# Performance work log

Measured on AMD Instinct MI355X. Metric: run time of the kernel, lower is better.

The kernel has to match this reference:

```python
import jax, jax.numpy as jnp
import numpy as np

B, L, H, D = 2, 2048, 16, 64
E = H * D  # 1024

def setup_inputs() -> dict:
    key = jax.random.key(0)
    k1, k2, k3 = jax.random.split(key, 3)
    net_in = jax.random.normal(k1, (B, L, E), dtype=jnp.float32)
    # torch nn.Linear weights are [out_features, in_features]; scale like kaiming-uniform-ish
    W_qkv = jax.random.normal(k2, (3 * E, E), dtype=jnp.float32) * (1.0 / np.sqrt(E))
    W_out = jax.random.normal(k3, (E, E), dtype=jnp.float32) * (1.0 / np.sqrt(E))
    return {"net_in": net_in, "W_qkv": W_qkv, "W_out": W_out}

def reference(net_in, W_qkv, W_out):
    b, l, c = net_in.shape
    h, d = H, D
    # c_proj: x @ W_qkv.T -> (B, L, 3E), split into q, k, v
    qkv = jnp.einsum('blc,ec->ble', net_in, W_qkv)
    q, k, v = jnp.split(qkv, 3, axis=-1)
    # reshape to (B, H, L, D)
    q = q.reshape(b, l, h, d).transpose(0, 2, 1, 3)
    k = k.reshape(b, l, h, d).transpose(0, 2, 1, 3)
    v = v.reshape(b, l, h, d).transpose(0, 2, 1, 3)
    scale = 1.0 / np.sqrt(d).astype(np.float32)
    attn = jnp.einsum('bhqd,bhkd->bhqk', q, k) * scale  # (B, H, L, L)
    causal = jnp.tril(jnp.ones((l, l), dtype=bool))
    attn = jnp.where(causal[None, None, :, :], attn, -jnp.inf)
    attn = jax.nn.softmax(attn, axis=-1)
    out = jnp.einsum('bhqk,bhkd->bhqd', attn, v)  # (B, H, L, D)
    out = out.transpose(0, 2, 1, 3).reshape(b, l, c)
    return jnp.einsum('blc,ec->ble', out, W_out)
```

## Files before the change

### kernel.cpp

```cpp
#include <hip/hip_runtime.h>
#include <hip/hip_bf16.h>

#define LOG2E 1.44269504088896340736f

typedef __attribute__((ext_vector_type(8))) short s16x8;
typedef __attribute__((ext_vector_type(4))) short s16x4;
typedef __attribute__((ext_vector_type(2))) unsigned int u32x2;
typedef __attribute__((ext_vector_type(4))) float f32x4;
typedef __attribute__((ext_vector_type(16))) float f32x16;

__device__ inline short f2bf(float f) {
  __hip_bfloat16 h = __float2bfloat16(f);
  union { __hip_bfloat16 h; short s; } u; u.h = h; return u.s;
}

__device__ inline void gl_lds16(const void* g, void* l) {
  __builtin_amdgcn_global_load_lds(
      (const __attribute__((address_space(1))) void*)g,
      (__attribute__((address_space(3))) void*)l, 16, 0, 0);
}

__global__ __launch_bounds__(256)
void cvt_all(const float* __restrict__ Wqkv, const float* __restrict__ Wout,
             const float* __restrict__ net,
             short* __restrict__ dWqkv, short* __restrict__ dWout,
             short* __restrict__ dnet) {
  int bid = blockIdx.x;
  const float* src; short* dst; int i;
  if (bid < 3072)      { src = Wqkv; dst = dWqkv; i = bid * 256 + threadIdx.x; }
  else if (bid < 4096) { src = Wout; dst = dWout; i = (bid - 3072) * 256 + threadIdx.x; }
  else                 { src = net;  dst = dnet;  i = (bid - 4096) * 256 + threadIdx.x; }
  f32x4 v = ((const f32x4*)src)[i];
  s16x4 o;
  o[0] = f2bf(v[0]); o[1] = f2bf(v[1]); o[2] = f2bf(v[2]); o[3] = f2bf(v[3]);
  ((s16x4*)dst)[i] = o;
}

template<int OUTF32, int VTRANS, int SPLITK, int NSUB>
__global__ __launch_bounds__(256)
void gemm128(const short* __restrict__ A, int lda,
             const short* __restrict__ B, int ldb,
             void* __restrict__ Cp, int ldc, int Klen,
             short* __restrict__ P1) {
  int id = (int)(blockIdx.x + (blockIdx.y << 5));
  int xcd = id & 7, slot = id >> 3;
  int m0, n0;
  if constexpr (NSUB == 3) {
    int g = slot / 12, r = slot - g * 12;
    m0 = (g * 4 + (r & 3)) * 128;
    n0 = (xcd * 3 + (r >> 2)) * 128;
  } else {
    m0 = (slot & 31) * 128;
    n0 = (xcd * NSUB + (slot >> 5)) * 128;
  }
  int kbeg = SPLITK ? (int)blockIdx.z * Klen : 0;
  int t = threadIdx.x;
  int w = t >> 6, lane = t & 63;
  int l16 = lane & 15, quad = lane >> 4;
  int wm = w >> 1, wn = w & 1;

  __shared__ __align__(16) short As[2][128 * 32];
  __shared__ __align__(16) short Bs[2][128 * 32];

  int scell = ((t & 3) ^ ((t >> 3) & 3)) * 8;
  const short* bsrc = B + (size_t)(n0 + (t >> 2)) * ldb + kbeg + scell;
  const short* asrc = A + (size_t)(m0 + (t >> 2)) * lda + kbeg + scell;
  int rcell = (quad ^ ((l16 >> 1) & 3)) * 8;

  f32x4 acc[4][4];
#pragma unroll
  for (int i = 0; i < 4; ++i)
#pragma unroll
    for (int j = 0; j < 4; ++j) acc[i][j] = (f32x4){0.f, 0.f, 0.f, 0.f};

#pragma unroll
  for (int r = 0; r < 2; ++r) {
    gl_lds16(asrc + (size_t)r * 64 * lda, (char*)As + r * 4096 + w * 1024);
    gl_lds16(bsrc + (size_t)r * 64 * ldb, (char*)Bs + r * 4096 + w * 1024);
  }

  int nks = Klen >> 5;
  for (int ks = 0; ks < nks; ++ks) {
    int cur = ks & 1;
    if (ks + 1 < nks) {
      int k0 = (ks + 1) * 32;
      int nb = cur ^ 1;
#pragma unroll
      for (int r = 0; r < 2; ++r) {
        gl_lds16(asrc + k0 + (size_t)r * 64 * lda, (char*)As + nb * 8192 + r * 4096 + w * 1024);
        gl_lds16(bsrc + k0 + (size_t)r * 64 * ldb, (char*)Bs + nb * 8192 + r * 4096 + w * 1024);
      }
      asm volatile("s_waitcnt vmcnt(4)" ::: "memory");
    } else {
      asm volatile("s_waitcnt vmcnt(0)" ::: "memory");
    }
    asm volatile("s_barrier" ::: "memory");

    s16x8 af[4], bf[4];
#pragma unroll
    for (int i = 0; i < 4; ++i) {
      af[i] = *(const s16x8*)(As[cur] + (wm * 64 + i * 16 + l16) * 32 + rcell);
      bf[i] = *(const s16x8*)(Bs[cur] + (wn * 64 + i * 16 + l16) * 32 + rcell);
    }
#pragma unroll
    for (int i = 0; i < 4; ++i)
#pragma unroll
      for (int j = 0; j < 4; ++j)
        acc[i][j] = __builtin_amdgcn_mfma_f32_16x16x32_bf16(af[i], bf[j], acc[i][j], 0, 0, 0);

    asm volatile("s_barrier" ::: "memory");
  }

  if (SPLITK && blockIdx.z == 1) {
#pragma unroll
    for (int i = 0; i < 4; ++i)
#pragma unroll
      for (int j = 0; j < 4; ++j)
#pragma unroll
        for (int rr = 0; rr < 4; ++rr) {
          size_t row = m0 + wm * 64 + i * 16 + quad * 4 + rr;
          size_t col = n0 + wn * 64 + j * 16 + l16;
          float* fp = (float*)(P1 + row * 3072 + 1024);
          fp[col] = acc[i][j][rr];
        }
  } else if (VTRANS && n0 >= 2048) {
    short* Cs = (short*)Cp;
#pragma unroll
    for (int i = 0; i < 4; ++i)
#pragma unroll
      for (int j = 0; j < 4; ++j) {
        int colg = n0 + wn * 64 + j * 16 + l16;
        int d = colg & 63;
        size_t dst = (size_t)(m0 + wm * 64 + d) * ldc + (colg - d) + i * 16 + quad * 4;
        s16x4 ob;
#pragma unroll
        for (int rr = 0; rr < 4; ++rr) ob[rr] = f2bf(acc[i][j][rr]);
        *(s16x4*)(Cs + dst) = ob;
      }
  } else {
#pragma unroll
    for (int i = 0; i < 4; ++i)
#pragma unroll
      for (int j = 0; j < 4; ++j)
#pragma unroll
        for (int rr = 0; rr < 4; ++rr) {
          size_t row = m0 + wm * 64 + i * 16 + quad * 4 + rr;
          size_t col = n0 + wn * 64 + j * 16 + l16;
          if (OUTF32) ((float*)Cp)[row * ldc + col] = acc[i][j][rr];
          else        ((short*)Cp)[row * ldc + col] = f2bf(acc[i][j][rr]);
        }
  }
}

__global__ __launch_bounds__(256)
void reduce_add(float* __restrict__ out, const short* __restrict__ qkv) {
  int row = blockIdx.x;
  int c = threadIdx.x;
  const f32x4* p = (const f32x4*)(qkv + (size_t)row * 3072 + 1024);
  f32x4* o = (f32x4*)(out + (size_t)row * 1024);
  f32x4 v = o[c];
  f32x4 q = p[c];
  v[0] += q[0]; v[1] += q[1]; v[2] += q[2]; v[3] += q[3];
  o[c] = v;
}

__global__ __launch_bounds__(256, 4)
void attn(short* __restrict__ qkv) {
  const int L = 2048, E3 = 3072, EO = 1024;
  int id = (int)(blockIdx.x + (blockIdx.y << 5));
  int xcd = id & 7;
  int s = id >> 3;
  int bh = xcd * 4 + (s & 3);
  int u = s >> 2;
  int vv = u & 15;
  int qidx = (u & 16) ? (31 - vv) : vv;
  int b = bh >> 4, h = bh & 15;
  int q0 = qidx * 64;
  int t = threadIdx.x;
  int wave = t >> 6, lane = t & 63;
  int qh = wave >> 1, kh = wave & 1;
  int l31 = lane & 31, hsel = lane >> 5;
  int khi4 = hsel * 4;
  int key = (lane >> 1) & 3;
  const float SENT = -3.0e38f;
  const float SC = 0.125f * LOG2E;

  __shared__ __align__(16) short Ks[2][2][64][32];
  __shared__ __align__(16) short Vt[2][2][64][32];

  int rowbase = b * L;

  s16x8 qf[4];
  {
    const short* qp = qkv + (size_t)(rowbase + q0 + qh * 32 + l31) * E3 + h * 64 + hsel * 8;
#pragma unroll
    for (int e = 0; e < 4; ++e) {
      s16x8 raw = *(const s16x8*)(qp + e * 16);
#pragma unroll
      for (int j = 0; j < 8; ++j) {
        union { float f; int i; } u2; u2.i = ((int)(unsigned short)raw[j]) << 16;
        raw[j] = f2bf(u2.f * SC);
      }
      qf[e] = raw;
    }
  }

  int scell = ((lane & 3) ^ ((lane >> 3) & 3)) * 8;
  const short* ksrc = qkv + (size_t)(rowbase + wave * 16 + (lane >> 2)) * E3 + EO
                      + h * 64 + scell;
  const short* vsrc = qkv + (size_t)(rowbase + wave * 16 + (lane >> 2)) * E3 + 2 * EO
                      + h * 64 + scell;

  float l_acc = 0.f;
  f32x16 o0 = (f32x16){0.f,0.f,0.f,0.f,0.f,0.f,0.f,0.f,0.f,0.f,0.f,0.f,0.f,0.f,0.f,0.f};
  f32x16 o1 = o0;

  int nkb = qidx + 1;

  gl_lds16(ksrc,      (char*)Ks + wave * 1024);
  gl_lds16(ksrc + 32, (char*)Ks + 4096 + wave * 1024);
  gl_lds16(vsrc,      (char*)Vt + wave * 1024);
  gl_lds16(vsrc + 32, (char*)Vt + 4096 + wave * 1024);

  for (int kb = 0; kb < nkb; ++kb) {
    int cur = kb & 1;
    __syncthreads();
    if (kb + 1 < nkb) {
      size_t koff = (size_t)((kb + 1) * 64) * E3;
      int nb = cur ^ 1;
      gl_lds16(ksrc + koff,      (char*)Ks + nb * 8192 + wave * 1024);
      gl_lds16(ksrc + koff + 32, (char*)Ks + nb * 8192 + 4096 + wave * 1024);
      gl_lds16(vsrc + koff,      (char*)Vt + nb * 8192 + wave * 1024);
      gl_lds16(vsrc + koff + 32, (char*)Vt + nb * 8192 + 4096 + wave * 1024);
    }

    int rel = (q0 + qh * 32) - (kb * 64 + kh * 32);
    if (rel > -32) {
      int krow = kh * 32 + l31;
      s16x8 kf0 = *(const s16x8*)(&Ks[cur][0][krow][((0 + hsel) ^ key) * 8]);
      s16x8 kf1 = *(const s16x8*)(&Ks[cur][0][krow][((2 + hsel) ^ key) * 8]);
      s16x8 kf2 = *(const s16x8*)(&Ks[cur][1][krow][((0 + hsel) ^ key) * 8]);
      s16x8 kf3 = *(const s16x8*)(&Ks[cur][1][krow][((2 + hsel) ^ key) * 8]);
      s16x8 vf00 = *(const s16x8*)(&Vt[cur][kh][ 0 + l31][((0 + hsel) ^ key) * 8]);
      s16x8 vf01 = *(const s16x8*)(&Vt[cur][kh][32 + l31][((0 + hsel) ^ key) * 8]);
      s16x8 vf10 = *(const s16x8*)(&Vt[cur][kh][ 0 + l31][((2 + hsel) ^ key) * 8]);
      s16x8 vf11 = *(const s16x8*)(&Vt[cur][kh][32 + l31][((2 + hsel) ^ key) * 8]);

      f32x16 sf = (f32x16){0.f,0.f,0.f,0.f,0.f,0.f,0.f,0.f,0.f,0.f,0.f,0.f,0.f,0.f,0.f,0.f};
      sf = __builtin_amdgcn_mfma_f32_32x32x16_bf16(kf0, qf[0], sf, 0, 0, 0);
      sf = __builtin_amdgcn_mfma_f32_32x32x16_bf16(kf1, qf[1], sf, 0, 0, 0);
      sf = __builtin_amdgcn_mfma_f32_32x32x16_bf16(kf2, qf[2], sf, 0, 0, 0);
      sf = __builtin_amdgcn_mfma_f32_32x32x16_bf16(kf3, qf[3], sf, 0, 0, 0);

      if (rel < 31) {
        int thr = rel + l31 - khi4;
#pragma unroll
        for (int r = 0; r < 16; ++r) {
          const int base_k = (r & 3) + 8 * (r >> 2);
          if (base_k > thr) sf[r] = SENT;
        }
      }

      float pv[16];
#pragma unroll
      for (int r = 0; r < 16; ++r) {
        pv[r] = __builtin_amdgcn_exp2f(sf[r]);
        l_acc += pv[r];
      }

#define PKW(lo, hi) __builtin_amdgcn_perm(__float_as_uint(hi) + 0x8000u, \
                                          __float_as_uint(lo) + 0x8000u, 0x07060302u)
      unsigned A0 = PKW(pv[0],  pv[1]),  A1 = PKW(pv[2],  pv[3]);
      unsigned B0 = PKW(pv[4],  pv[5]),  B1 = PKW(pv[6],  pv[7]);
      unsigned C0 = PKW(pv[8],  pv[9]),  C1 = PKW(pv[10], pv[11]);
      unsigned D0 = PKW(pv[12], pv[13]), D1 = PKW(pv[14], pv[15]);
#undef PKW
      u32x2 sw0 = __builtin_amdgcn_permlane32_swap(A0, B0, false, false);
      u32x2 sw1 = __builtin_amdgcn_permlane32_swap(A1, B1, false, false);
      u32x2 sw2 = __builtin_amdgcn_permlane32_swap(C0, D0, false, false);
      u32x2 sw3 = __builtin_amdgcn_permlane32_swap(C1, D1, false, false);
      union { s16x8 v; unsigned u[4]; } P0, P1;
      P0.u[0] = sw0[0]; P0.u[1] = sw1[0]; P0.u[2] = sw0[1]; P0.u[3] = sw1[1];
      P1.u[0] = sw2[0]; P1.u[1] = sw3[0]; P1.u[2] = sw2[1]; P1.u[3] = sw3[1];

      o0 = __builtin_amdgcn_mfma_f32_32x32x16_bf16(vf00, P0.v, o0, 0, 0, 0);
      o0 = __builtin_amdgcn_mfma_f32_32x32x16_bf16(vf10, P1.v, o0, 0, 0, 0);
      o1 = __builtin_amdgcn_mfma_f32_32x32x16_bf16(vf01, P0.v, o1, 0, 0, 0);
      o1 = __builtin_amdgcn_mfma_f32_32x32x16_bf16(vf11, P1.v, o1, 0, 0, 0);
    }
  }

  l_acc += __shfl_xor(l_acc, 32);
  __syncthreads();
  float* fs = (float*)&Ks[0][0][0][0];
  float* lb = (float*)&Vt[0][0][0][0];
  if (kh) {
#pragma unroll
    for (int r = 0; r < 16; ++r) {
      fs[qh * 2048 + r * 64 + lane] = o0[r];
      fs[qh * 2048 + (16 + r) * 64 + lane] = o1[r];
    }
    if (lane < 32) lb[qh * 32 + lane] = l_acc;
  }
  __syncthreads();
  if (!kh) {
    float inv = 1.f / (l_acc + lb[qh * 32 + l31]);
    size_t obase = (size_t)(rowbase + q0 + qh * 32 + l31) * E3 + h * 64;
    int fb = qh * 2048;
#pragma unroll
    for (int g = 0; g < 4; ++g) {
      s16x4 w0, w1;
#pragma unroll
      for (int rr = 0; rr < 4; ++rr) {
        int r = g * 4 + rr;
        w0[rr] = f2bf((o0[r] + fs[fb + r * 64 + lane]) * inv);
        w1[rr] = f2bf((o1[r] + fs[fb + (16 + r) * 64 + lane]) * inv);
      }
      *(s16x4*)(qkv + obase + g * 8 + khi4) = w0;
      *(s16x4*)(qkv + obase + 32 + g * 8 + khi4) = w1;
    }
  }
}

extern "C" void kernel_launch(void* const* d_in, const int* in_sizes, int n_in,
                              void* d_out, int out_size, void* d_ws, size_t ws_size,
                              hipStream_t stream) {
  const float* net_in = (const float*)d_in[0];
  const float* W_qkv  = (const float*)d_in[1];
  const float* W_out  = (const float*)d_in[2];

  short* Wqkvb = (short*)d_ws;
  short* Woutb = Wqkvb + (size_t)3072 * 1024;
  short* qkv   = Woutb + (size_t)1024 * 1024;
  short* netb  = (short*)d_out;

  cvt_all<<<8192, 256, 0, stream>>>(W_qkv, W_out, net_in, Wqkvb, Woutb, netb);

  gemm128<0, 1, 0, 3><<<dim3(32, 24), 256, 0, stream>>>(netb, 1024, Wqkvb, 1024,
                                                        qkv, 3072, 1024, nullptr);
  attn<<<dim3(32, 32), 256, 0, stream>>>(qkv);
  gemm128<1, 0, 1, 1><<<dim3(32, 8, 2), 256, 0, stream>>>(qkv, 3072, Woutb, 1024,
                                                          d_out, 1024, 512, qkv);
  reduce_add<<<4096, 256, 0, stream>>>((float*)d_out, qkv);
}
```

Baseline: 174.2 us.

## Switch GEMM to 32x32x16 MFMA tiles and use hardware bf16 pack in attention

Rewrites the 128x128 GEMM inner loop to use 32x32x16 bf16 MFMAs with 2x2 accumulators per wave instead of 16x16x32 with 4x4. This halves the fragment loads per step and raises MFMA efficiency, with matching changes to the LDS swizzle reads and the epilogue index maps. The explicit vmcnt waits are replaced by __syncthreads. In attention, the add-and-permute bf16 packing becomes v_cvt_pk_bf16_f32, which rounds to nearest-even and takes fewer instructions.

```diff
diff --git a/kernel.cpp b/kernel.cpp
--- a/kernel.cpp
+++ b/kernel.cpp
@@ -12,6 +12,12 @@
 __device__ inline short f2bf(float f) {
   __hip_bfloat16 h = __float2bfloat16(f);
   union { __hip_bfloat16 h; short s; } u; u.h = h; return u.s;
+}
+
+__device__ inline unsigned cvtpk(float lo, float hi) {
+  unsigned r;
+  asm("v_cvt_pk_bf16_f32 %0, %1, %2" : "=v"(r) : "v"(lo), "v"(hi));
+  return r;
 }
 
 __device__ inline void gl_lds16(const void* g, void* l) {
@@ -56,8 +62,9 @@
   int kbeg = SPLITK ? (int)blockIdx.z * Klen : 0;
   int t = threadIdx.x;
   int w = t >> 6, lane = t & 63;
-  int l16 = lane & 15, quad = lane >> 4;
+  int l31 = lane & 31, hsel = lane >> 5;
   int wm = w >> 1, wn = w & 1;
+  int key = (lane >> 1) & 3;
 
   __shared__ __align__(16) short As[2][128 * 32];
   __shared__ __align__(16) short Bs[2][128 * 32];
@@ -65,19 +72,20 @@
   int scell = ((t & 3) ^ ((t >> 3) & 3)) * 8;
   const short* bsrc = B + (size_t)(n0 + (t >> 2)) * ldb + kbeg + scell;
   const short* asrc = A + (size_t)(m0 + (t >> 2)) * lda + kbeg + scell;
-  int rcell = (quad ^ ((l16 >> 1) & 3)) * 8;
-
-  f32x4 acc[4][4];
-#pragma unroll
-  for (int i = 0; i < 4; ++i)
-#pragma unroll
-    for (int j = 0; j < 4; ++j) acc[i][j] = (f32x4){0.f, 0.f, 0.f, 0.f};
+
+  f32x16 acc[2][2];
+#pragma unroll
+  for (int i = 0; i < 2; ++i)
+#pragma unroll
+    for (int j = 0; j < 2; ++j)
+      acc[i][j] = (f32x16){0.f,0.f,0.f,0.f,0.f,0.f,0.f,0.f,0.f,0.f,0.f,0.f,0.f,0.f,0.f,0.f};
 
 #pragma unroll
   for (int r = 0; r < 2; ++r) {
     gl_lds16(asrc + (size_t)r * 64 * lda, (char*)As + r * 4096 + w * 1024);
     gl_lds16(bsrc + (size_t)r * 64 * ldb, (char*)Bs + r * 4096 + w * 1024);
   }
+  __syncthreads();
 
   int nks = Klen >> 5;
   for (int ks = 0; ks < nks; ++ks) {
@@ -90,64 +98,67 @@
         gl_lds16(asrc + k0 + (size_t)r * 64 * lda, (char*)As + nb * 8192 + r * 4096 + w * 1024);
         gl_lds16(bsrc + k0 + (size_t)r * 64 * ldb, (char*)Bs + nb * 8192 + r * 4096 + w * 1024);
       }
-      asm volatile("s_waitcnt vmcnt(4)" ::: "memory");
-    } else {
-      asm volatile("s_waitcnt vmcnt(0)" ::: "memory");
-    }
-    asm volatile("s_barrier" ::: "memory");
-
-    s16x8 af[4], bf[4];
-#pragma unroll
-    for (int i = 0; i < 4; ++i) {
-      af[i] = *(const s16x8*)(As[cur] + (wm * 64 + i * 16 + l16) * 32 + rcell);
-      bf[i] = *(const s16x8*)(Bs[cur] + (wn * 64 + i * 16 + l16) * 32 + rcell);
-    }
-#pragma unroll
-    for (int i = 0; i < 4; ++i)
-#pragma unroll
-      for (int j = 0; j < 4; ++j)
-        acc[i][j] = __builtin_amdgcn_mfma_f32_16x16x32_bf16(af[i], bf[j], acc[i][j], 0, 0, 0);
-
-    asm volatile("s_barrier" ::: "memory");
+    }
+
+    s16x8 af[2][2], bf[2][2];
+#pragma unroll
+    for (int ah = 0; ah < 2; ++ah)
+#pragma unroll
+      for (int kc = 0; kc < 2; ++kc) {
+        af[ah][kc] = *(const s16x8*)(As[cur] + (wm * 64 + ah * 32 + l31) * 32
+                                     + (((kc * 2 + hsel) ^ key) * 8));
+        bf[ah][kc] = *(const s16x8*)(Bs[cur] + (wn * 64 + ah * 32 + l31) * 32
+                                     + (((kc * 2 + hsel) ^ key) * 8));
+      }
+#pragma unroll
+    for (int ah = 0; ah < 2; ++ah)
+#pragma unroll
+      for (int bh = 0; bh < 2; ++bh) {
+        acc[ah][bh] = __builtin_amdgcn_mfma_f32_32x32x16_bf16(af[ah][0], bf[bh][0], acc[ah][bh], 0, 0, 0);
+        acc[ah][bh] = __builtin_amdgcn_mfma_f32_32x32x16_bf16(af[ah][1], bf[bh][1], acc[ah][bh], 0, 0, 0);
+      }
+
+    __syncthreads();
   }
 
   if (SPLITK && blockIdx.z == 1) {
 #pragma unroll
-    for (int i = 0; i < 4; ++i)
-#pragma unroll
-      for (int j = 0; j < 4; ++j)
-#pragma unroll
-        for (int rr = 0; rr < 4; ++rr) {
-          size_t row = m0 + wm * 64 + i * 16 + quad * 4 + rr;
-          size_t col = n0 + wn * 64 + j * 16 + l16;
-          float* fp = (float*)(P1 + row * 3072 + 1024);
-          fp[col] = acc[i][j][rr];
+    for (int ah = 0; ah < 2; ++ah)
+#pragma unroll
+      for (int bh = 0; bh < 2; ++bh)
+#pragma unroll
+        for (int r = 0; r < 16; ++r) {
+          size_t row = m0 + wm * 64 + ah * 32 + (r & 3) + 8 * (r >> 2) + 4 * hsel;
+          size_t col = n0 + wn * 64 + bh * 32 + l31;
+          ((float*)(P1 + row * 3072 + 1024))[col] = acc[ah][bh][r];
         }
   } else if (VTRANS && n0 >= 2048) {
     short* Cs = (short*)Cp;
 #pragma unroll
-    for (int i = 0; i < 4; ++i)
-#pragma unroll
-      for (int j = 0; j < 4; ++j) {
-        int colg = n0 + wn * 64 + j * 16 + l16;
-        int d = colg & 63;
-        size_t dst = (size_t)(m0 + wm * 64 + d) * ldc + (colg - d) + i * 16 + quad * 4;
-        s16x4 ob;
-#pragma unroll
-        for (int rr = 0; rr < 4; ++rr) ob[rr] = f2bf(acc[i][j][rr]);
-        *(s16x4*)(Cs + dst) = ob;
+    for (int ah = 0; ah < 2; ++ah)
+#pragma unroll
+      for (int bh = 0; bh < 2; ++bh) {
+        int d = bh * 32 + l31;
+        size_t base = (size_t)(m0 + wm * 64 + d) * ldc + (n0 + wn * 64);
+#pragma unroll
+        for (int g = 0; g < 4; ++g) {
+          s16x4 ob;
+#pragma unroll
+          for (int rr = 0; rr < 4; ++rr) ob[rr] = f2bf(acc[ah][bh][g * 4 + rr]);
+          *(s16x4*)(Cs + base + ah * 32 + g * 8 + 4 * hsel) = ob;
+        }
       }
   } else {
 #pragma unroll
-    for (int i = 0; i < 4; ++i)
-#pragma unroll
-      for (int j = 0; j < 4; ++j)
-#pragma unroll
-        for (int rr = 0; rr < 4; ++rr) {
-          size_t row = m0 + wm * 64 + i * 16 + quad * 4 + rr;
-          size_t col = n0 + wn * 64 + j * 16 + l16;
-          if (OUTF32) ((float*)Cp)[row * ldc + col] = acc[i][j][rr];
-          else        ((short*)Cp)[row * ldc + col] = f2bf(acc[i][j][rr]);
+    for (int ah = 0; ah < 2; ++ah)
+#pragma unroll
+      for (int bh = 0; bh < 2; ++bh)
+#pragma unroll
+        for (int r = 0; r < 16; ++r) {
+          size_t row = m0 + wm * 64 + ah * 32 + (r & 3) + 8 * (r >> 2) + 4 * hsel;
+          size_t col = n0 + wn * 64 + bh * 32 + l31;
+          if (OUTF32) ((float*)Cp)[row * ldc + col] = acc[ah][bh][r];
+          else        ((short*)Cp)[row * ldc + col] = f2bf(acc[ah][bh][r]);
         }
   }
 }
@@ -268,13 +279,10 @@
         l_acc += pv[r];
       }
 
-#define PKW(lo, hi) __builtin_amdgcn_perm(__float_as_uint(hi) + 0x8000u, \
-                                          __float_as_uint(lo) + 0x8000u, 0x07060302u)
-      unsigned A0 = PKW(pv[0],  pv[1]),  A1 = PKW(pv[2],  pv[3]);
-      unsigned B0 = PKW(pv[4],  pv[5]),  B1 = PKW(pv[6],  pv[7]);
-      unsigned C0 = PKW(pv[8],  pv[9]),  C1 = PKW(pv[10], pv[11]);
-      unsigned D0 = PKW(pv[12], pv[13]), D1 = PKW(pv[14], pv[15]);
-#undef PKW
+      unsigned A0 = cvtpk(pv[0],  pv[1]),  A1 = cvtpk(pv[2],  pv[3]);
+      unsigned B0 = cvtpk(pv[4],  pv[5]),  B1 = cvtpk(pv[6],  pv[7]);
+      unsigned C0 = cvtpk(pv[8],  pv[9]),  C1 = cvtpk(pv[10], pv[11]);
+      unsigned D0 = cvtpk(pv[12], pv[13]), D1 = cvtpk(pv[14], pv[15]);
       u32x2 sw0 = __builtin_amdgcn_permlane32_swap(A0, B0, false, false);
       u32x2 sw1 = __builtin_amdgcn_permlane32_swap(A1, B1, false, false);
       u32x2 sw2 = __builtin_amdgcn_permlane32_swap(C0, D0, false, false);
```

After: 177.4 us. No clear change (+1.8%).
